# Kernel tuning notes

Measured on AMD Instinct MI355X. Metric: run time of the kernel, lower is better.

## Reference

```python
import jax, jax.numpy as jnp
import numpy as np

NUM_GRAPHS = 512

def setup_inputs() -> dict:
    key = jax.random.key(0)
    ks = jax.random.split(key, 16)
    N, E, F_IN, D = 50000, 800000, 128, 64
    x = jax.random.normal(ks[0], (N, F_IN), dtype=jnp.float32)
    edge_index = jax.random.randint(ks[1], (2, E), 0, N, dtype=jnp.int32)
    batch_index = jnp.sort(jax.random.randint(ks[2], (N,), 0, NUM_GRAPHS, dtype=jnp.int32))
    def lin(k, fin, fout):
        s = 1.0 / np.sqrt(fin)
        return jax.random.uniform(k, (fin, fout), jnp.float32, -s, s)
    return {
        "x": x, "edge_index": edge_index, "batch_index": batch_index,
        "W0": lin(ks[3], F_IN, D), "b0": jnp.zeros((D,), jnp.float32),
        "W1": lin(ks[4], D, D), "b1": jnp.zeros((D,), jnp.float32),
        "W2": lin(ks[5], D, D), "b2": jnp.zeros((D,), jnp.float32),
        "W3": lin(ks[6], D, D), "b3": jnp.zeros((D,), jnp.float32),
        "Wout": lin(ks[7], 2 * D, 1), "bout": jnp.zeros((1,), jnp.float32),
    }

def _gcn_edges(edge_index, N):
    # add self-loops and compute symmetric normalization D^-1/2 (A+I) D^-1/2
    loops = jnp.arange(N, dtype=edge_index.dtype)
    row = jnp.concatenate([edge_index[0], loops])  # source
    col = jnp.concatenate([edge_index[1], loops])  # target
    deg = jax.ops.segment_sum(jnp.ones_like(col, dtype=jnp.float32), col, num_segments=N)
    dinv = jnp.where(deg > 0, jax.lax.rsqrt(deg), 0.0)
    norm = dinv[row] * dinv[col]  # [E+N]
    return row, col, norm

def _gcn_conv(h, row, col, norm, W, b, N):
    h = h @ W                                   # [N, D] linear transform first
    msg = h[row] * norm[:, None]                # gather + scale
    out = jax.ops.segment_sum(msg, col, num_segments=N)  # scatter-add
    return out + b

def reference(x, edge_index, batch_index, W0, b0, W1, b1, W2, b2, W3, b3, Wout, bout):
    N = x.shape[0]
    row, col, norm = _gcn_edges(edge_index, N)
    h = jnp.tanh(_gcn_conv(x, row, col, norm, W0, b0, N))
    h = jnp.tanh(_gcn_conv(h, row, col, norm, W1, b1, N))
    h = jnp.tanh(_gcn_conv(h, row, col, norm, W2, b2, N))
    h = jnp.tanh(_gcn_conv(h, row, col, norm, W3, b3, N))
    gmax = jax.ops.segment_max(h, batch_index, num_segments=NUM_GRAPHS)
    gmax = jnp.where(jnp.isfinite(gmax), gmax, 0.0)  # empty segments -> 0
    gsum = jax.ops.segment_sum(h, batch_index, num_segments=NUM_GRAPHS)
    cnt = jax.ops.segment_sum(jnp.ones((N,), jnp.float32), batch_index, num_segments=NUM_GRAPHS)
    gmean = gsum / jnp.maximum(cnt, 1.0)[:, None]
    hidden = jnp.concatenate([gmax, gmean], axis=1)   # [G, 2D]
    out = hidden @ Wout + bout                        # [G, 1]
    return out, hidden
```

## Files before the change

### kernel.cpp

```cpp
#include <hip/hip_runtime.h>
#include <hip/hip_fp16.h>
#include <math.h>

#define CAP 64
typedef unsigned short ushort_t;
typedef unsigned int uint_t;

__device__ inline float4 f4add(float4 a, float4 b) {
    return make_float4(a.x + b.x, a.y + b.y, a.z + b.z, a.w + b.w);
}

__device__ inline float4 h4tof4(uint2 u) {
    __half2 lo = *reinterpret_cast<__half2*>(&u.x);
    __half2 hi = *reinterpret_cast<__half2*>(&u.y);
    float2 a = __half22float2(lo);
    float2 b = __half22float2(hi);
    return make_float4(a.x, a.y, b.x, b.y);
}

__device__ inline uint_t packh2(float a, float b) {
    __half2 h = __floats2half2_rn(a, b);
    return *reinterpret_cast<uint_t*>(&h);
}

__global__ __launch_bounds__(256) void k_scatter2(const int* __restrict__ row,
                                                  const int* __restrict__ col, int E, int N,
                                                  int* __restrict__ deg, ushort_t* __restrict__ csr) {
    const int part = blockIdx.x & 7;
    const int slot = blockIdx.x >> 3;
    const int nslots = gridDim.x >> 3;
    const int lo = (int)((long long)N * part / 8);
    const int hi = (int)((long long)N * (part + 1) / 8);
    const int nq = E >> 2;
    for (int t = slot * blockDim.x + threadIdx.x; t < nq; t += nslots * blockDim.x) {
        int4 c = ((const int4*)col)[t];
        int4 r = ((const int4*)row)[t];
        if (c.x >= lo && c.x < hi) { int d = atomicAdd(&deg[c.x], 1); if (d < CAP) csr[((size_t)c.x << 6) + d] = (ushort_t)r.x; }
        if (c.y >= lo && c.y < hi) { int d = atomicAdd(&deg[c.y], 1); if (d < CAP) csr[((size_t)c.y << 6) + d] = (ushort_t)r.y; }
        if (c.z >= lo && c.z < hi) { int d = atomicAdd(&deg[c.z], 1); if (d < CAP) csr[((size_t)c.z << 6) + d] = (ushort_t)r.z; }
        if (c.w >= lo && c.w < hi) { int d = atomicAdd(&deg[c.w], 1); if (d < CAP) csr[((size_t)c.w << 6) + d] = (ushort_t)r.w; }
    }
    if (blockIdx.x == 0) {
        for (int e = (nq << 2) + threadIdx.x; e < E; e += blockDim.x) {
            int c = col[e];
            int d = atomicAdd(&deg[c], 1);
            if (d < CAP) csr[((size_t)c << 6) + d] = (ushort_t)row[e];
        }
    }
}

template <int K>
__global__ __launch_bounds__(256) void k_gemm(const float* __restrict__ X,
                                              const float* __restrict__ W,
                                              const int* __restrict__ deg,
                                              ushort_t* __restrict__ Gbh, int N) {
    __shared__ __align__(16) float Wl[32 * 64];
    __shared__ __align__(16) float Xl[64 * 36];

    const int tid = threadIdx.x;
    const int wave = tid >> 6, lane = tid & 63;
    const int d8 = lane & 7, ns = lane >> 3;
    const int n0 = wave * 16 + ns, n1 = n0 + 8;

    const int base = blockIdx.x * 64;
    if (base >= N) return;
    const int tile_n = min(64, N - base);

    float4 a0l = {0,0,0,0}, a0h = {0,0,0,0}, a1l = {0,0,0,0}, a1h = {0,0,0,0};

    for (int kh = 0; kh < K / 32; kh++) {
        __syncthreads();
        for (int i = tid; i < 512; i += 256)
            ((float4*)Wl)[i] = ((const float4*)(W + kh * 2048))[i];
        for (int idx = tid; idx < 512; idx += 256) {
            int n = idx >> 3, q = idx & 7;
            float4 v = {0,0,0,0};
            if (n < tile_n) v = ((const float4*)(X + (size_t)(base + n) * K + kh * 32))[q];
            ((float4*)(Xl + n * 36))[q] = v;
        }
        __syncthreads();

        const float4* xq0 = (const float4*)(Xl + n0 * 36);
        const float4* xq1 = (const float4*)(Xl + n1 * 36);
        const float* wcol = Wl + d8 * 8;
#pragma unroll
        for (int kq = 0; kq < 8; kq++) {
            const float4 x4a = xq0[kq];
            const float4 x4b = xq1[kq];
            const float xs0[4] = {x4a.x, x4a.y, x4a.z, x4a.w};
            const float xs1[4] = {x4b.x, x4b.y, x4b.z, x4b.w};
#pragma unroll
            for (int j = 0; j < 4; j++) {
                const int k = kq * 4 + j;
                const float4 wa = *(const float4*)(wcol + k * 64);
                const float4 wb = *(const float4*)(wcol + k * 64 + 4);
                const float xa = xs0[j];
                const float xb = xs1[j];
                a0l.x = fmaf(xa, wa.x, a0l.x); a0l.y = fmaf(xa, wa.y, a0l.y);
                a0l.z = fmaf(xa, wa.z, a0l.z); a0l.w = fmaf(xa, wa.w, a0l.w);
                a0h.x = fmaf(xa, wb.x, a0h.x); a0h.y = fmaf(xa, wb.y, a0h.y);
                a0h.z = fmaf(xa, wb.z, a0h.z); a0h.w = fmaf(xa, wb.w, a0h.w);
                a1l.x = fmaf(xb, wa.x, a1l.x); a1l.y = fmaf(xb, wa.y, a1l.y);
                a1l.z = fmaf(xb, wa.z, a1l.z); a1l.w = fmaf(xb, wa.w, a1l.w);
                a1h.x = fmaf(xb, wb.x, a1h.x); a1h.y = fmaf(xb, wb.y, a1h.y);
                a1h.z = fmaf(xb, wb.z, a1h.z); a1h.w = fmaf(xb, wb.w, a1h.w);
            }
        }
    }

    int gn0 = base + n0, gn1 = base + n1;
    if (gn0 < N) {
        float s = rsqrtf((float)(deg[gn0] + 1));
        uint4 o;
        o.x = packh2(a0l.x * s, a0l.y * s);
        o.y = packh2(a0l.z * s, a0l.w * s);
        o.z = packh2(a0h.x * s, a0h.y * s);
        o.w = packh2(a0h.z * s, a0h.w * s);
        ((uint4*)(Gbh + (size_t)gn0 * 64))[d8] = o;
    }
    if (gn1 < N) {
        float s = rsqrtf((float)(deg[gn1] + 1));
        uint4 o;
        o.x = packh2(a1l.x * s, a1l.y * s);
        o.y = packh2(a1l.z * s, a1l.w * s);
        o.z = packh2(a1h.x * s, a1h.y * s);
        o.w = packh2(a1h.z * s, a1h.w * s);
        ((uint4*)(Gbh + (size_t)gn1 * 64))[d8] = o;
    }
}

__global__ __launch_bounds__(512) void k_agg_gemm(const ushort_t* __restrict__ Gin,
                                                  const int* __restrict__ deg,
                                                  const ushort_t* __restrict__ csr,
                                                  const float* __restrict__ bias,
                                                  const float* __restrict__ W,
                                                  ushort_t* __restrict__ Gout, int N) {
    __shared__ __align__(16) float Wl[64 * 64];
    __shared__ __align__(16) float Hl[32 * 68];

    const int tid = threadIdx.x;
    const int wave = tid >> 6, lane = tid & 63;
    const int base = blockIdx.x * 32;
    if (base >= N) return;

    ((float4*)Wl)[tid]       = ((const float4*)W)[tid];
    ((float4*)Wl)[tid + 512] = ((const float4*)W)[tid + 512];

    const int s = lane >> 4;
    const int q = lane & 15;
    const int ln = wave * 4 + s;
    const int n = base + ln;
    const bool alive = (n < N);

    int cnt = 0;
    if (alive) { cnt = deg[n]; if (cnt > CAP) cnt = CAP; }
    const ushort_t* rowp = csr + ((size_t)(alive ? n : 0) << 6);

    uint4 ia = {0,0,0,0}, ib = {0,0,0,0}, ic = {0,0,0,0}, idd = {0,0,0,0};
    if (cnt > 0)  ia  = *(const uint4*)(rowp);
    if (cnt > 8)  ib  = *(const uint4*)(rowp + 8);
    if (cnt > 16) ic  = *(const uint4*)(rowp + 16);
    if (cnt > 24) idd = *(const uint4*)(rowp + 24);

    float4 acc = {0.f, 0.f, 0.f, 0.f};
    if (alive) acc = h4tof4(((const uint2*)(Gin + (size_t)n * 64))[q]);

    const uint_t iw[16] = {ia.x, ia.y, ia.z, ia.w, ib.x, ib.y, ib.z, ib.w,
                           ic.x, ic.y, ic.z, ic.w, idd.x, idd.y, idd.z, idd.w};
#pragma unroll
    for (int h = 0; h < 2; h++) {
        const int hb = h * 16;
        uint2 hv[16];
#pragma unroll
        for (int m = 0; m < 8; m++) {
            const uint_t u = iw[h * 8 + m];
            const int j0 = u & 0xffff, j1 = u >> 16;
            uint2 a = {0u, 0u}, b = {0u, 0u};
            if (hb + 2 * m < cnt)     a = ((const uint2*)(Gin + (size_t)j0 * 64))[q];
            if (hb + 2 * m + 1 < cnt) b = ((const uint2*)(Gin + (size_t)j1 * 64))[q];
            hv[2 * m] = a;
            hv[2 * m + 1] = b;
        }
        float4 t0 = f4add(h4tof4(hv[0]),  h4tof4(hv[1]));
        float4 t1 = f4add(h4tof4(hv[2]),  h4tof4(hv[3]));
        float4 t2 = f4add(h4tof4(hv[4]),  h4tof4(hv[5]));
        float4 t3 = f4add(h4tof4(hv[6]),  h4tof4(hv[7]));
        float4 t4 = f4add(h4tof4(hv[8]),  h4tof4(hv[9]));
        float4 t5 = f4add(h4tof4(hv[10]), h4tof4(hv[11]));
        float4 t6 = f4add(h4tof4(hv[12]), h4tof4(hv[13]));
        float4 t7 = f4add(h4tof4(hv[14]), h4tof4(hv[15]));
        float4 u0 = f4add(t0, t1), u1 = f4add(t2, t3);
        float4 u2 = f4add(t4, t5), u3 = f4add(t6, t7);
        acc = f4add(acc, f4add(f4add(u0, u1), f4add(u2, u3)));
    }
    for (int i = 32; i < cnt; i += 2) {
        const uint_t u = *(const uint_t*)(rowp + i);
        const int j0 = u & 0xffff;
        acc = f4add(acc, h4tof4(((const uint2*)(Gin + (size_t)j0 * 64))[q]));
        if (i + 1 < cnt) {
            const int j1 = u >> 16;
            acc = f4add(acc, h4tof4(((const uint2*)(Gin + (size_t)j1 * 64))[q]));
        }
    }

    float4 r4 = {0.f, 0.f, 0.f, 0.f};
    if (alive) {
        float dinv = rsqrtf((float)(cnt + 1));
        float4 b4 = ((const float4*)bias)[q];
        r4.x = tanhf(fmaf(acc.x, dinv, b4.x));
        r4.y = tanhf(fmaf(acc.y, dinv, b4.y));
        r4.z = tanhf(fmaf(acc.z, dinv, b4.z));
        r4.w = tanhf(fmaf(acc.w, dinv, b4.w));
    }
    ((float4*)(Hl + ln * 68))[q] = r4;

    __syncthreads();

    const int gn = tid >> 4;
    const int qd = tid & 15;
    const float* hrow = Hl + gn * 68;
    const float* wcol = Wl + qd * 4;
    float4 o = {0.f, 0.f, 0.f, 0.f};
#pragma unroll
    for (int k = 0; k < 64; k++) {
        const float x = hrow[k];
        const float4 w4 = *(const float4*)(wcol + k * 64);
        o.x = fmaf(x, w4.x, o.x);
        o.y = fmaf(x, w4.y, o.y);
        o.z = fmaf(x, w4.z, o.z);
        o.w = fmaf(x, w4.w, o.w);
    }
    const int gnode = base + gn;
    if (gnode < N) {
        float sc = rsqrtf((float)(deg[gnode] + 1));
        uint2 u2o;
        u2o.x = packh2(o.x * sc, o.y * sc);
        u2o.y = packh2(o.z * sc, o.w * sc);
        ((uint2*)(Gout + (size_t)gnode * 64))[qd] = u2o;
    }
}

__global__ __launch_bounds__(256) void k_agg(const ushort_t* __restrict__ Gbh,
                                             const int* __restrict__ deg,
                                             const ushort_t* __restrict__ csr,
                                             const float* __restrict__ bias,
                                             float* __restrict__ H, int N) {
    const int tid = threadIdx.x;
    const int wave = tid >> 6, lane = tid & 63;
    const int s = lane >> 4;
    const int q = lane & 15;
    const int n = blockIdx.x * 16 + wave * 4 + s;
    const bool alive = (n < N);

    int cnt = 0;
    if (alive) { cnt = deg[n]; if (cnt > CAP) cnt = CAP; }
    const ushort_t* rowp = csr + ((size_t)(alive ? n : 0) << 6);

    uint4 ia = {0,0,0,0}, ib = {0,0,0,0}, ic = {0,0,0,0}, idd = {0,0,0,0};
    if (cnt > 0)  ia  = *(const uint4*)(rowp);
    if (cnt > 8)  ib  = *(const uint4*)(rowp + 8);
    if (cnt > 16) ic  = *(const uint4*)(rowp + 16);
    if (cnt > 24) idd = *(const uint4*)(rowp + 24);

    float4 acc = {0.f, 0.f, 0.f, 0.f};
    if (alive) acc = h4tof4(((const uint2*)(Gbh + (size_t)n * 64))[q]);

    const uint_t iw[16] = {ia.x, ia.y, ia.z, ia.w, ib.x, ib.y, ib.z, ib.w,
                           ic.x, ic.y, ic.z, ic.w, idd.x, idd.y, idd.z, idd.w};

#pragma unroll
    for (int h = 0; h < 2; h++) {
        const int hb = h * 16;
        uint2 hv[16];
#pragma unroll
        for (int m = 0; m < 8; m++) {
            const uint_t u = iw[h * 8 + m];
            const int j0 = u & 0xffff, j1 = u >> 16;
            uint2 a = {0u, 0u}, b = {0u, 0u};
            if (hb + 2 * m < cnt)     a = ((const uint2*)(Gbh + (size_t)j0 * 64))[q];
            if (hb + 2 * m + 1 < cnt) b = ((const uint2*)(Gbh + (size_t)j1 * 64))[q];
            hv[2 * m] = a;
            hv[2 * m + 1] = b;
        }
        float4 t0 = f4add(h4tof4(hv[0]),  h4tof4(hv[1]));
        float4 t1 = f4add(h4tof4(hv[2]),  h4tof4(hv[3]));
        float4 t2 = f4add(h4tof4(hv[4]),  h4tof4(hv[5]));
        float4 t3 = f4add(h4tof4(hv[6]),  h4tof4(hv[7]));
        float4 t4 = f4add(h4tof4(hv[8]),  h4tof4(hv[9]));
        float4 t5 = f4add(h4tof4(hv[10]), h4tof4(hv[11]));
        float4 t6 = f4add(h4tof4(hv[12]), h4tof4(hv[13]));
        float4 t7 = f4add(h4tof4(hv[14]), h4tof4(hv[15]));
        float4 u0 = f4add(t0, t1), u1 = f4add(t2, t3);
        float4 u2 = f4add(t4, t5), u3 = f4add(t6, t7);
        acc = f4add(acc, f4add(f4add(u0, u1), f4add(u2, u3)));
    }

    for (int i = 32; i < cnt; i += 2) {
        const uint_t u = *(const uint_t*)(rowp + i);
        const int j0 = u & 0xffff;
        acc = f4add(acc, h4tof4(((const uint2*)(Gbh + (size_t)j0 * 64))[q]));
        if (i + 1 < cnt) {
            const int j1 = u >> 16;
            acc = f4add(acc, h4tof4(((const uint2*)(Gbh + (size_t)j1 * 64))[q]));
        }
    }

    if (alive) {
        float dinv = rsqrtf((float)(cnt + 1));
        float4 b4 = ((const float4*)bias)[q];
        float4 r;
        r.x = tanhf(fmaf(acc.x, dinv, b4.x));
        r.y = tanhf(fmaf(acc.y, dinv, b4.y));
        r.z = tanhf(fmaf(acc.z, dinv, b4.z));
        r.w = tanhf(fmaf(acc.w, dinv, b4.w));
        ((float4*)(H + (size_t)n * 64))[q] = r;
    }
}

__global__ __launch_bounds__(256) void k_pool(const float* __restrict__ H,
                                              const int* __restrict__ batch, int N, int Gn,
                                              const float* __restrict__ Wout,
                                              const float* __restrict__ bout,
                                              float* __restrict__ out,
                                              float* __restrict__ hidden) {
    __shared__ float lm[4][64];
    __shared__ float ls[4][64];
    const int g = blockIdx.x;
    if (g >= Gn) return;
    const int tid = threadIdx.x;
    const int w = tid >> 6, lane = tid & 63;

    int lo = 0, hi = N;
    while (lo < hi) { int m = (lo + hi) >> 1; if (batch[m] < g) lo = m + 1; else hi = m; }
    const int s = lo;
    hi = N;
    while (lo < hi) { int m = (lo + hi) >> 1; if (batch[m] < g + 1) lo = m + 1; else hi = m; }
    const int c = lo - s;
    const int e = s + c;

    float m0 = -INFINITY, m1 = -INFINITY, m2 = -INFINITY, m3 = -INFINITY;
    float s0 = 0.f, s1 = 0.f, s2 = 0.f, s3 = 0.f;
    int n = s + w;
    for (; n + 12 < e; n += 16) {
        float v0 = H[(size_t)n * 64 + lane];
        float v1 = H[(size_t)(n + 4) * 64 + lane];
        float v2 = H[(size_t)(n + 8) * 64 + lane];
        float v3 = H[(size_t)(n + 12) * 64 + lane];
        m0 = fmaxf(m0, v0); s0 += v0;
        m1 = fmaxf(m1, v1); s1 += v1;
        m2 = fmaxf(m2, v2); s2 += v2;
        m3 = fmaxf(m3, v3); s3 += v3;
    }
    for (; n < e; n += 4) {
        float v = H[(size_t)n * 64 + lane];
        m0 = fmaxf(m0, v); s0 += v;
    }
    lm[w][lane] = fmaxf(fmaxf(m0, m1), fmaxf(m2, m3));
    ls[w][lane] = (s0 + s1) + (s2 + s3);
    __syncthreads();
    if (w == 0) {
        float vmax = fmaxf(fmaxf(lm[0][lane], lm[1][lane]), fmaxf(lm[2][lane], lm[3][lane]));
        float vsum = (ls[0][lane] + ls[1][lane]) + (ls[2][lane] + ls[3][lane]);
        float gmax = (c > 0) ? vmax : 0.f;
        float gmean = (c > 0) ? vsum / (float)c : 0.f;
        hidden[(size_t)g * 128 + lane] = gmax;
        hidden[(size_t)g * 128 + 64 + lane] = gmean;
        float p = fmaf(gmax, Wout[lane], gmean * Wout[64 + lane]);
        for (int o = 32; o > 0; o >>= 1) p += __shfl_down(p, o);
        if (lane == 0) out[g] = p + bout[0];
    }
}

extern "C" void kernel_launch(void* const* d_in, const int* in_sizes, int n_in,
                              void* d_out, int out_size, void* d_ws, size_t ws_size,
                              hipStream_t stream) {
    const float* x    = (const float*)d_in[0];
    const int*   ei   = (const int*)d_in[1];
    const int*   batch= (const int*)d_in[2];
    const float* W0 = (const float*)d_in[3];  const float* b0 = (const float*)d_in[4];
    const float* W1 = (const float*)d_in[5];  const float* b1 = (const float*)d_in[6];
    const float* W2 = (const float*)d_in[7];  const float* b2 = (const float*)d_in[8];
    const float* W3 = (const float*)d_in[9];  const float* b3 = (const float*)d_in[10];
    const float* Wout = (const float*)d_in[11]; const float* bout = (const float*)d_in[12];

    const int N  = in_sizes[2];
    const int E  = in_sizes[1] / 2;
    const int Gn = out_size / 129;

    const int* row = ei;
    const int* col = ei + E;

    float* out_p    = (float*)d_out;
    float* hidden_p = out_p + Gn;

    char* wp = (char*)d_ws;
    auto alloc = [&](size_t bytes) { void* p = (void*)wp; wp += (bytes + 255) & ~(size_t)255; return p; };
    int*      deg = (int*)alloc((size_t)N * 4);
    ushort_t* csr = (ushort_t*)alloc((size_t)N * CAP * 2);
    ushort_t* Ga  = (ushort_t*)alloc((size_t)N * 64 * 2);
    ushort_t* Gc  = (ushort_t*)alloc((size_t)N * 64 * 2);
    float*    Hb  = (float*)alloc((size_t)N * 64 * 4);

    hipMemsetAsync(deg, 0, (size_t)N * 4, stream);
    k_scatter2<<<2048, 256, 0, stream>>>(row, col, E, N, deg, csr);

    const int gblocks  = (N + 63) / 64;
    const int fblocks  = (N + 31) / 32;
    const int ablocks  = (N + 15) / 16;

    k_gemm<128><<<gblocks, 256, 0, stream>>>(x, W0, deg, Ga, N);
    k_agg_gemm<<<fblocks, 512, 0, stream>>>(Ga, deg, csr, b0, W1, Gc, N);
    k_agg_gemm<<<fblocks, 512, 0, stream>>>(Gc, deg, csr, b1, W2, Ga, N);
    k_agg_gemm<<<fblocks, 512, 0, stream>>>(Ga, deg, csr, b2, W3, Gc, N);
    k_agg<<<ablocks, 256, 0, stream>>>(Gc, deg, csr, b3, Hb, N);

    k_pool<<<Gn, 256, 0, stream>>>(Hb, batch, N, Gn, Wout, bout, out_p, hidden_p);
}
```

Measured before the change: 276.1 us.

## Fuse final aggregation with graph pooling via global atomics and last-block finalize

Merges the last aggregation kernel with the pooling kernel. Each node's tanh output is pushed straight into per-graph max and sum buffers with atomics, and a last-arriving block computes hidden and the output projection. This removes writing and re-reading the full fp32 node feature buffer and one kernel launch. In exchange it adds heavy atomic contention on a small set of addresses, a serial finalize pass in one block, and order-dependent float sums.

Measured after the change: 745.3 us. 170% more time.

```diff
diff --git a/kernel.cpp b/kernel.cpp
--- a/kernel.cpp
+++ b/kernel.cpp
@@ -21,6 +21,15 @@
 __device__ inline uint_t packh2(float a, float b) {
     __half2 h = __floats2half2_rn(a, b);
     return *reinterpret_cast<uint_t*>(&h);
+}
+
+__device__ inline uint_t fkey(float f) {
+    uint_t b = __float_as_uint(f);
+    return (b & 0x80000000u) ? ~b : (b | 0x80000000u);
+}
+__device__ inline float fdecode(uint_t k) {
+    uint_t b = (k & 0x80000000u) ? (k & 0x7FFFFFFFu) : ~k;
+    return __uint_as_float(b);
 }
 
 __global__ __launch_bounds__(256) void k_scatter2(const int* __restrict__ row,
@@ -240,11 +249,18 @@
     }
 }
 
-__global__ __launch_bounds__(256) void k_agg(const ushort_t* __restrict__ Gbh,
-                                             const int* __restrict__ deg,
-                                             const ushort_t* __restrict__ csr,
-                                             const float* __restrict__ bias,
-                                             float* __restrict__ H, int N) {
+__global__ __launch_bounds__(256) void k_agg_pool(const ushort_t* __restrict__ Gbh,
+                                                  const int* __restrict__ deg,
+                                                  const ushort_t* __restrict__ csr,
+                                                  const float* __restrict__ bias,
+                                                  const int* __restrict__ batch, int N, int Gn,
+                                                  const float* __restrict__ Wout,
+                                                  const float* __restrict__ bout,
+                                                  float* __restrict__ out,
+                                                  float* __restrict__ hidden,
+                                                  uint_t* __restrict__ pmax,
+                                                  float* __restrict__ psum,
+                                                  int* __restrict__ done) {
     const int tid = threadIdx.x;
     const int wave = tid >> 6, lane = tid & 63;
     const int s = lane >> 4;
@@ -313,61 +329,40 @@
         r.y = tanhf(fmaf(acc.y, dinv, b4.y));
         r.z = tanhf(fmaf(acc.z, dinv, b4.z));
         r.w = tanhf(fmaf(acc.w, dinv, b4.w));
-        ((float4*)(H + (size_t)n * 64))[q] = r;
-    }
-}
-
-__global__ __launch_bounds__(256) void k_pool(const float* __restrict__ H,
-                                              const int* __restrict__ batch, int N, int Gn,
-                                              const float* __restrict__ Wout,
-                                              const float* __restrict__ bout,
-                                              float* __restrict__ out,
-                                              float* __restrict__ hidden) {
-    __shared__ float lm[4][64];
-    __shared__ float ls[4][64];
-    const int g = blockIdx.x;
-    if (g >= Gn) return;
-    const int tid = threadIdx.x;
-    const int w = tid >> 6, lane = tid & 63;
-
-    int lo = 0, hi = N;
-    while (lo < hi) { int m = (lo + hi) >> 1; if (batch[m] < g) lo = m + 1; else hi = m; }
-    const int s = lo;
-    hi = N;
-    while (lo < hi) { int m = (lo + hi) >> 1; if (batch[m] < g + 1) lo = m + 1; else hi = m; }
-    const int c = lo - s;
-    const int e = s + c;
-
-    float m0 = -INFINITY, m1 = -INFINITY, m2 = -INFINITY, m3 = -INFINITY;
-    float s0 = 0.f, s1 = 0.f, s2 = 0.f, s3 = 0.f;
-    int n = s + w;
-    for (; n + 12 < e; n += 16) {
-        float v0 = H[(size_t)n * 64 + lane];
-        float v1 = H[(size_t)(n + 4) * 64 + lane];
-        float v2 = H[(size_t)(n + 8) * 64 + lane];
-        float v3 = H[(size_t)(n + 12) * 64 + lane];
-        m0 = fmaxf(m0, v0); s0 += v0;
-        m1 = fmaxf(m1, v1); s1 += v1;
-        m2 = fmaxf(m2, v2); s2 += v2;
-        m3 = fmaxf(m3, v3); s3 += v3;
-    }
-    for (; n < e; n += 4) {
-        float v = H[(size_t)n * 64 + lane];
-        m0 = fmaxf(m0, v); s0 += v;
-    }
-    lm[w][lane] = fmaxf(fmaxf(m0, m1), fmaxf(m2, m3));
-    ls[w][lane] = (s0 + s1) + (s2 + s3);
+        const int gid = batch[n];
+        uint_t* pm = pmax + (size_t)gid * 64 + q * 4;
+        float*  ps = psum + (size_t)gid * 64 + q * 4;
+        atomicMax(pm + 0, fkey(r.x)); atomicAdd(ps + 0, r.x);
+        atomicMax(pm + 1, fkey(r.y)); atomicAdd(ps + 1, r.y);
+        atomicMax(pm + 2, fkey(r.z)); atomicAdd(ps + 2, r.z);
+        atomicMax(pm + 3, fkey(r.w)); atomicAdd(ps + 3, r.w);
+    }
+
+    __threadfence();
+    __shared__ int ticket;
+    if (tid == 0) ticket = atomicAdd(done, 1);
     __syncthreads();
-    if (w == 0) {
-        float vmax = fmaxf(fmaxf(lm[0][lane], lm[1][lane]), fmaxf(lm[2][lane], lm[3][lane]));
-        float vsum = (ls[0][lane] + ls[1][lane]) + (ls[2][lane] + ls[3][lane]);
-        float gmax = (c > 0) ? vmax : 0.f;
-        float gmean = (c > 0) ? vsum / (float)c : 0.f;
-        hidden[(size_t)g * 128 + lane] = gmax;
-        hidden[(size_t)g * 128 + 64 + lane] = gmean;
-        float p = fmaf(gmax, Wout[lane], gmean * Wout[64 + lane]);
-        for (int o = 32; o > 0; o >>= 1) p += __shfl_down(p, o);
-        if (lane == 0) out[g] = p + bout[0];
+
+    if (ticket == (int)gridDim.x - 1) {
+        for (int g = tid; g < Gn; g += blockDim.x) {
+            int lo = 0, hi = N;
+            while (lo < hi) { int m = (lo + hi) >> 1; if (batch[m] < g) lo = m + 1; else hi = m; }
+            const int seg = lo;
+            hi = N;
+            while (lo < hi) { int m = (lo + hi) >> 1; if (batch[m] < g + 1) lo = m + 1; else hi = m; }
+            const int c = lo - seg;
+            float acco = 0.f;
+            for (int d = 0; d < 64; d++) {
+                uint_t k = atomicOr(&pmax[(size_t)g * 64 + d], 0u);
+                float  sm = atomicAdd(&psum[(size_t)g * 64 + d], 0.0f);
+                float mx = 0.f, mn = 0.f;
+                if (c > 0) { mx = fdecode(k); mn = sm / (float)c; }
+                hidden[(size_t)g * 128 + d] = mx;
+                hidden[(size_t)g * 128 + 64 + d] = mn;
+                acco += mx * Wout[d] + mn * Wout[64 + d];
+            }
+            out[g] = acco + bout[0];
+        }
     }
 }
 
@@ -395,24 +390,26 @@
 
     char* wp = (char*)d_ws;
     auto alloc = [&](size_t bytes) { void* p = (void*)wp; wp += (bytes + 255) & ~(size_t)255; return p; };
-    int*      deg = (int*)alloc((size_t)N * 4);
-    ushort_t* csr = (ushort_t*)alloc((size_t)N * CAP * 2);
-    ushort_t* Ga  = (ushort_t*)alloc((size_t)N * 64 * 2);
-    ushort_t* Gc  = (ushort_t*)alloc((size_t)N * 64 * 2);
-    float*    Hb  = (float*)alloc((size_t)N * 64 * 4);
-
-    hipMemsetAsync(deg, 0, (size_t)N * 4, stream);
+    int*      deg  = (int*)alloc((size_t)N * 4);
+    uint_t*   pmax = (uint_t*)alloc((size_t)Gn * 64 * 4);
+    float*    psum = (float*)alloc((size_t)Gn * 64 * 4);
+    int*      done = (int*)alloc(256);
+    ushort_t* csr  = (ushort_t*)alloc((size_t)N * CAP * 2);
+    ushort_t* Ga   = (ushort_t*)alloc((size_t)N * 64 * 2);
+    ushort_t* Gc   = (ushort_t*)alloc((size_t)N * 64 * 2);
+
+    const size_t zbytes = (size_t)((char*)done - (char*)deg) + 256;
+    hipMemsetAsync(deg, 0, zbytes, stream);
     k_scatter2<<<2048, 256, 0, stream>>>(row, col, E, N, deg, csr);
 
-    const int gblocks  = (N + 63) / 64;
-    const int fblocks  = (N + 31) / 32;
-    const int ablocks  = (N + 15) / 16;
+    const int gblocks = (N + 63) / 64;
+    const int fblocks = (N + 31) / 32;
+    const int ablocks = (N + 15) / 16;
 
     k_gemm<128><<<gblocks, 256, 0, stream>>>(x, W0, deg, Ga, N);
     k_agg_gemm<<<fblocks, 512, 0, stream>>>(Ga, deg, csr, b0, W1, Gc, N);
     k_agg_gemm<<<fblocks, 512, 0, stream>>>(Gc, deg, csr, b1, W2, Ga, N);
     k_agg_gemm<<<fblocks, 512, 0, stream>>>(Ga, deg, csr, b2, W3, Gc, N);
-    k_agg<<<ablocks, 256, 0, stream>>>(Gc, deg, csr, b3, Hb, N);
-
-    k_pool<<<Gn, 256, 0, stream>>>(Hb, batch, N, Gn, Wout, bout, out_p, hidden_p);
-}
+    k_agg_pool<<<ablocks, 256, 0, stream>>>(Gc, deg, csr, b3, batch, N, Gn,
+                                            Wout, bout, out_p, hidden_p, pmax, psum, done);
+}
```
